# Kernel tuning notes

Hardware: AMD Instinct MI355X
Metric: run time of the kernel (lower is better)

## Reference

```python
import jax, jax.numpy as jnp
import numpy as np

N = 20000
E = 640000
IN_C, HID_C, OUT_C = 256, 256, 128
R = 8


def setup_inputs() -> dict:
    key = jax.random.key(0)
    ks = jax.random.split(key, 10)
    x = jax.random.normal(ks[0], (N, IN_C), dtype=jnp.float32)
    edge_index = jax.random.randint(ks[1], (2, E), 0, N, dtype=jnp.int64)
    edge_type = jax.random.randint(ks[2], (E,), 0, R, dtype=jnp.int64)
    s1 = 1.0 / np.sqrt(IN_C)
    s2 = 1.0 / np.sqrt(HID_C)
    W1 = jax.random.normal(ks[3], (R, IN_C, HID_C), dtype=jnp.float32) * s1
    root1 = jax.random.normal(ks[4], (IN_C, HID_C), dtype=jnp.float32) * s1
    b1 = jnp.zeros((HID_C,), dtype=jnp.float32)
    W2 = jax.random.normal(ks[5], (R, HID_C, OUT_C), dtype=jnp.float32) * s2
    root2 = jax.random.normal(ks[6], (HID_C, OUT_C), dtype=jnp.float32) * s2
    b2 = jnp.zeros((OUT_C,), dtype=jnp.float32)
    return {"x": x, "W1": W1, "root1": root1, "b1": b1,
            "W2": W2, "root2": root2, "b2": b2,
            "edge_index": edge_index, "edge_type": edge_type}


def _rgcn_conv(x, W, root, b, src, dst, etype):
    # Per-relation transform of ALL nodes: [R, N, out]
    t = jnp.einsum('ni,rio->rno', x, W)
    # Gather relation-specific messages per edge: [E, out]
    msg = t[etype, src]
    # Mean aggregation per (target node, relation), as in PyG RGCNConv (aggr='mean')
    comp = dst * R + etype  # composite segment id [E]
    cnt = jax.ops.segment_sum(jnp.ones_like(etype, dtype=x.dtype), comp,
                              num_segments=x.shape[0] * R)
    norm = 1.0 / jnp.maximum(cnt[comp], 1.0)
    agg = jax.ops.segment_sum(msg * norm[:, None], dst,
                              num_segments=x.shape[0])
    return agg + x @ root + b


def reference(x, W1, root1, b1, W2, root2, b2, edge_index, edge_type):
    src, dst = edge_index[0], edge_index[1]
    h = jax.nn.relu(_rgcn_conv(x, W1, root1, b1, src, dst, edge_type))
    return _rgcn_conv(h, W2, root2, b2, src, dst, edge_type)
```

## Files before the change

kernel.cpp:

```cpp
#include <hip/hip_runtime.h>

#define NN 20000
#define NE 640000
#define NR 8
#define NSEG (NN * NR)
#define KCAT 2304
#define KA   2048
#define CH1 256
#define CH2 128

typedef __attribute__((ext_vector_type(8))) short short8;
typedef __attribute__((ext_vector_type(4))) float f32x4;

#define AS_GLOBAL __attribute__((address_space(1)))
#define AS_LDS    __attribute__((address_space(3)))

__device__ __forceinline__ float bf2f(unsigned short u) {
    unsigned int x = ((unsigned int)u) << 16;
    return __builtin_bit_cast(float, x);
}
__device__ __forceinline__ unsigned short f2bf(float f) {
    unsigned int u = __builtin_bit_cast(unsigned int, f);
    u = (u + 0x7FFFu + ((u >> 16) & 1u)) >> 16;
    return (unsigned short)u;
}
__device__ __forceinline__ f32x4 cvt4(ushort4 v) {
    f32x4 r;
    r.x = bf2f(v.x); r.y = bf2f(v.y); r.z = bf2f(v.z); r.w = bf2f(v.w);
    return r;
}

__global__ void prologue1(const int* __restrict__ dst, const int* __restrict__ et,
                          int* __restrict__ cnt,
                          const float* __restrict__ x, unsigned short* __restrict__ xbf) {
    int gid = blockIdx.x * 256 + threadIdx.x;
    if (gid < NN * 64) {
        float4 v = reinterpret_cast<const float4*>(x)[gid];
        ushort4 o;
        o.x = f2bf(v.x); o.y = f2bf(v.y); o.z = f2bf(v.z); o.w = f2bf(v.w);
        reinterpret_cast<ushort4*>(xbf)[gid] = o;
    }
    if (gid < NE) atomicAdd(&cnt[et[gid] * NN + dst[gid]], 1);
}

__global__ void scan1(const int* __restrict__ cnt, int* __restrict__ off,
                      int* __restrict__ bsum) {
    __shared__ int s[256];
    int i = blockIdx.x * 256 + threadIdx.x;
    int v = (i < NSEG) ? cnt[i] : 0;
    s[threadIdx.x] = v;
    __syncthreads();
    for (int d = 1; d < 256; d <<= 1) {
        int t = (threadIdx.x >= d) ? s[threadIdx.x - d] : 0;
        __syncthreads();
        s[threadIdx.x] += t;
        __syncthreads();
    }
    if (i < NSEG) off[i] = s[threadIdx.x] - v;
    if (threadIdx.x == 255) bsum[blockIdx.x] = s[255];
}

__global__ __launch_bounds__(1024) void scan2(int* __restrict__ bsum, int nb) {
    __shared__ int s[1024];
    int t = threadIdx.x;
    int v = (t < nb) ? bsum[t] : 0;
    s[t] = v;
    __syncthreads();
    for (int d = 1; d < 1024; d <<= 1) {
        int tv = (t >= d) ? s[t - d] : 0;
        __syncthreads();
        s[t] += tv;
        __syncthreads();
    }
    if (t < nb) bsum[t] = s[t] - v;
}

__global__ void scan3(int* __restrict__ off, const int* __restrict__ bsum,
                      int* __restrict__ cursor) {
    int i = blockIdx.x * 256 + threadIdx.x;
    if (i < NSEG) {
        int o = off[i] + bsum[blockIdx.x];
        off[i] = o;
        cursor[i] = o;
    }
}

__global__ void bucket_kernel(const int* __restrict__ src, const int* __restrict__ dst,
                              const int* __restrict__ et, int* __restrict__ cursor,
                              int* __restrict__ ss) {
    int e = blockIdx.x * blockDim.x + threadIdx.x;
    if (e < NE) {
        int p = atomicAdd(&cursor[et[e] * NN + dst[e]], 1);
        ss[p] = src[e];
    }
}

__global__ void build_wt_all(const float* __restrict__ root1, const float* __restrict__ W1,
                             const float* __restrict__ root2, const float* __restrict__ W2,
                             unsigned short* __restrict__ W1T, unsigned short* __restrict__ W2T) {
    int i = blockIdx.x * 256 + threadIdx.x;
    if (i < CH1 * KCAT) {
        int n = i / KCAT, k = i - n * KCAT;
        float v = (k < 256) ? root1[(size_t)k * CH1 + n] : W1[(size_t)(k - 256) * CH1 + n];
        W1T[(size_t)n * KCAT + k] = f2bf(v);
    } else if (i < (CH1 + CH2) * KCAT) {
        int j = i - CH1 * KCAT;
        int n = j / KCAT, k = j - n * KCAT;
        float v = (k < 256) ? root2[(size_t)k * CH2 + n] : W2[(size_t)(k - 256) * CH2 + n];
        W2T[(size_t)n * KCAT + k] = f2bf(v);
    }
}

__global__ __launch_bounds__(256) void gather_all(const unsigned short* __restrict__ xb,
                                                  const int* __restrict__ ss,
                                                  const int* __restrict__ off,
                                                  const int* __restrict__ cnt,
                                                  unsigned short* __restrict__ A,
                                                  int n0, int rows) {
    int wid  = blockIdx.x * 4 + (threadIdx.x >> 6);
    int lane = threadIdx.x & 63;
    if (wid >= rows * NR) return;
    int n = wid >> 3;
    int r = wid & 7;
    int idx  = r * NN + (n0 + n);
    int base = off[idx];
    int c    = cnt[idx];

    f32x4 z = {0.f, 0.f, 0.f, 0.f};
    f32x4 a0 = z, a1 = z, a2 = z, a3 = z;
    int jj = 0;
    for (; jj + 4 <= c; jj += 4) {
        int s0 = ss[base + jj + 0];
        int s1 = ss[base + jj + 1];
        int s2 = ss[base + jj + 2];
        int s3 = ss[base + jj + 3];
        ushort4 v0 = reinterpret_cast<const ushort4*>(xb + (size_t)s0 * 256)[lane];
        ushort4 v1 = reinterpret_cast<const ushort4*>(xb + (size_t)s1 * 256)[lane];
        ushort4 v2 = reinterpret_cast<const ushort4*>(xb + (size_t)s2 * 256)[lane];
        ushort4 v3 = reinterpret_cast<const ushort4*>(xb + (size_t)s3 * 256)[lane];
        a0 += cvt4(v0); a1 += cvt4(v1); a2 += cvt4(v2); a3 += cvt4(v3);
    }
    int rem = c - jj;
    if (rem > 0) {
        int s0 = ss[base + jj + 0];
        int s1 = (rem > 1) ? ss[base + jj + 1] : s0;
        int s2 = (rem > 2) ? ss[base + jj + 2] : s0;
        ushort4 v0 = reinterpret_cast<const ushort4*>(xb + (size_t)s0 * 256)[lane];
        ushort4 v1 = (rem > 1) ? reinterpret_cast<const ushort4*>(xb + (size_t)s1 * 256)[lane] : make_ushort4(0,0,0,0);
        ushort4 v2 = (rem > 2) ? reinterpret_cast<const ushort4*>(xb + (size_t)s2 * 256)[lane] : make_ushort4(0,0,0,0);
        a0 += cvt4(v0);
        if (rem > 1) a1 += cvt4(v1);
        if (rem > 2) a2 += cvt4(v2);
    }
    f32x4 acc = (a0 + a1) + (a2 + a3);
    float inv = (c > 0) ? 1.f / (float)c : 0.f;
    ushort4 o;
    o.x = f2bf(acc.x * inv); o.y = f2bf(acc.y * inv);
    o.z = f2bf(acc.z * inv); o.w = f2bf(acc.w * inv);
    reinterpret_cast<ushort4*>(A + (size_t)n * KA + r * 256)[lane] = o;
}

template<int NOUT, int BN, bool RELU_BF16>
__global__ __launch_bounds__(256) void gemm_mfma(const unsigned short* __restrict__ A,
                                                 const unsigned short* __restrict__ Xsrc,
                                                 const unsigned short* __restrict__ BT,
                                                 const float* __restrict__ bias,
                                                 void* __restrict__ Cout,
                                                 int M, int mrow0) {
    constexpr int MI = 2;
    constexpr int NI = BN / 32;
    __shared__ __align__(16) unsigned short As[64 * 64];
    __shared__ __align__(16) unsigned short Bs[BN * 64];
    const int tid  = threadIdx.x;
    const int lane = tid & 63;
    const int w    = tid >> 6;
    const int wr   = w >> 1, wc = w & 1;
    const int wrow = wr * 32;
    const int wcol = wc * (NI * 16);
    const int row0 = blockIdx.x * 64;
    const int col0 = blockIdx.y * BN;

    const int srow8 = lane >> 3;
    const int skk8  = (lane & 7) * 8;
    int ra0 = row0 + w * 16 + srow8;
    int ra1 = row0 + w * 16 + 8 + srow8;
    ra0 = (ra0 < M) ? ra0 : (M - 1);
    ra1 = (ra1 < M) ? ra1 : (M - 1);
    const unsigned short* pax0 = Xsrc + (size_t)(mrow0 + ra0) * 256 + skk8;
    const unsigned short* pax1 = Xsrc + (size_t)(mrow0 + ra1) * 256 + skk8;
    const unsigned short* paa0 = A + (size_t)ra0 * KA + skk8 - 256;
    const unsigned short* paa1 = A + (size_t)ra1 * KA + skk8 - 256;
    unsigned short* lA0 = As + (w * 16) * 64;
    unsigned short* lA1 = As + (w * 16 + 8) * 64;
    constexpr int BI = BN / 32;
    const unsigned short* pb[4];
    unsigned short* lB[4];
    #pragma unroll
    for (int i = 0; i < BI; ++i) {
        int rb = (BN == 128) ? (w * 32 + i * 8) : (w * 16 + i * 8);
        pb[i] = BT + (size_t)(col0 + rb + srow8) * KCAT + skk8;
        lB[i] = Bs + (rb) * 64;
    }

    f32x4 acc[MI][NI] = {};
    const int fr = lane & 15;
    const int ka = (lane >> 4) * 8;

    for (int k0 = 0; k0 < KCAT; k0 += 64) {
        const unsigned short* p0 = (k0 < 256) ? (pax0 + k0) : (paa0 + k0);
        const unsigned short* p1 = (k0 < 256) ? (pax1 + k0) : (paa1 + k0);
        __builtin_amdgcn_global_load_lds((const AS_GLOBAL unsigned int*)p0,
                                         (AS_LDS unsigned int*)lA0, 16, 0, 0);
        __builtin_amdgcn_global_load_lds((const AS_GLOBAL unsigned int*)p1,
                                         (AS_LDS unsigned int*)lA1, 16, 0, 0);
        #pragma unroll
        for (int i = 0; i < BI; ++i)
            __builtin_amdgcn_global_load_lds((const AS_GLOBAL unsigned int*)(pb[i] + k0),
                                             (AS_LDS unsigned int*)lB[i], 16, 0, 0);
        __syncthreads();

        short8 af[MI][2], bfr[NI][2];
        #pragma unroll
        for (int i = 0; i < MI; ++i) {
            af[i][0] = *reinterpret_cast<const short8*>(&As[(wrow + i * 16 + fr) * 64 + ka]);
            af[i][1] = *reinterpret_cast<const short8*>(&As[(wrow + i * 16 + fr) * 64 + 32 + ka]);
        }
        #pragma unroll
        for (int i = 0; i < NI; ++i) {
            bfr[i][0] = *reinterpret_cast<const short8*>(&Bs[(wcol + i * 16 + fr) * 64 + ka]);
            bfr[i][1] = *reinterpret_cast<const short8*>(&Bs[(wcol + i * 16 + fr) * 64 + 32 + ka]);
        }
        #pragma unroll
        for (int s = 0; s < 2; ++s)
            #pragma unroll
            for (int mi = 0; mi < MI; ++mi)
                #pragma unroll
                for (int ni = 0; ni < NI; ++ni)
                    acc[mi][ni] = __builtin_amdgcn_mfma_f32_16x16x32_bf16(af[mi][s], bfr[ni][s], acc[mi][ni], 0, 0, 0);
        __syncthreads();
    }

    #pragma unroll
    for (int mi = 0; mi < MI; ++mi) {
        #pragma unroll
        for (int q = 0; q < 4; ++q) {
            int gm = row0 + wrow + mi * 16 + (lane >> 4) * 4 + q;
            if (gm >= M) continue;
            #pragma unroll
            for (int ni = 0; ni < NI; ++ni) {
                int gn = col0 + wcol + ni * 16 + fr;
                float v = acc[mi][ni][q] + bias[gn];
                if (RELU_BF16) {
                    v = fmaxf(v, 0.f);
                    ((unsigned short*)Cout)[(size_t)(mrow0 + gm) * NOUT + gn] = f2bf(v);
                } else {
                    ((float*)Cout)[(size_t)(mrow0 + gm) * NOUT + gn] = v;
                }
            }
        }
    }
}

extern "C" void kernel_launch(void* const* d_in, const int* in_sizes, int n_in,
                              void* d_out, int out_size, void* d_ws, size_t ws_size,
                              hipStream_t stream) {
    const float* x     = (const float*)d_in[0];
    const float* W1    = (const float*)d_in[1];
    const float* root1 = (const float*)d_in[2];
    const float* b1    = (const float*)d_in[3];
    const float* W2    = (const float*)d_in[4];
    const float* root2 = (const float*)d_in[5];
    const float* b2    = (const float*)d_in[6];
    const int*   ei    = (const int*)d_in[7];
    const int*   et    = (const int*)d_in[8];
    const int* src = ei;
    const int* dst = ei + NE;
    float* out = (float*)d_out;

    char* ws = (char*)d_ws;
    int*            cnt    = (int*)(ws + 0);
    int*            off    = (int*)(ws + 640000);
    int*            cursor = (int*)(ws + 1280000);
    int*            bsum   = (int*)(ws + 1920000);
    int*            ss     = (int*)(ws + 1923072);
    unsigned short* x_bf   = (unsigned short*)(ws + 4483072);
    unsigned short* h_bf   = (unsigned short*)(ws + 14723072);
    unsigned short* W1T    = (unsigned short*)(ws + 24963072);
    unsigned short* W2T    = (unsigned short*)(ws + 26142720);
    unsigned short* A      = (unsigned short*)(ws + 26732544);

    size_t availA = (ws_size > 26732544) ? ws_size - 26732544 : 0;
    int rowsC = (int)(availA / ((size_t)KA * 2));
    if (rowsC > NN) rowsC = NN;
    if (rowsC >= 256) rowsC &= ~127;
    if (rowsC < 1) rowsC = 1;

    const int NB = (NSEG + 255) / 256;

    hipMemsetAsync(cnt, 0, (size_t)NSEG * 4, stream);
    prologue1<<<(NN * 64 + 255) / 256, 256, 0, stream>>>(dst, et, cnt, x, x_bf);
    scan1<<<NB, 256, 0, stream>>>(cnt, off, bsum);
    scan2<<<1, 1024, 0, stream>>>(bsum, NB);
    scan3<<<NB, 256, 0, stream>>>(off, bsum, cursor);
    bucket_kernel<<<(NE + 255) / 256, 256, 0, stream>>>(src, dst, et, cursor, ss);
    build_wt_all<<<((CH1 + CH2) * KCAT + 255) / 256, 256, 0, stream>>>(root1, W1, root2, W2, W1T, W2T);

    for (int n0 = 0; n0 < NN; n0 += rowsC) {
        int rows = (NN - n0 < rowsC) ? (NN - n0) : rowsC;
        gather_all<<<(rows * NR + 3) / 4, 256, 0, stream>>>(x_bf, ss, off, cnt, A, n0, rows);
        dim3 g((rows + 63) / 64, CH1 / 128);
        gemm_mfma<CH1, 128, true><<<g, 256, 0, stream>>>(A, x_bf, W1T, b1, h_bf, rows, n0);
    }
    for (int n0 = 0; n0 < NN; n0 += rowsC) {
        int rows = (NN - n0 < rowsC) ? (NN - n0) : rowsC;
        gather_all<<<(rows * NR + 3) / 4, 256, 0, stream>>>(h_bf, ss, off, cnt, A, n0, rows);
        dim3 g((rows + 63) / 64, CH2 / 64);
        gemm_mfma<CH2, 64, false><<<g, 256, 0, stream>>>(A, h_bf, W2T, b2, out, rows, n0);
    }
}
```

Measured before the change: 419.2 us.

## Double-buffer GEMM LDS tiles and XOR-swizzle columns to avoid bank conflicts

```diff
diff --git a/kernel.cpp b/kernel.cpp
--- a/kernel.cpp
+++ b/kernel.cpp
@@ -169,8 +169,10 @@
                                                  int M, int mrow0) {
     constexpr int MI = 2;
     constexpr int NI = BN / 32;
-    __shared__ __align__(16) unsigned short As[64 * 64];
-    __shared__ __align__(16) unsigned short Bs[BN * 64];
+    constexpr int BI = BN / 32;
+    constexpr int NT = KCAT / 64;
+    __shared__ __align__(16) unsigned short As[2][64 * 64];
+    __shared__ __align__(16) unsigned short Bs[2][BN * 64];
     const int tid  = threadIdx.x;
     const int lane = tid & 63;
     const int w    = tid >> 6;
@@ -181,54 +183,69 @@
     const int col0 = blockIdx.y * BN;
 
     const int srow8 = lane >> 3;
-    const int skk8  = (lane & 7) * 8;
+    const int csw   = ((lane & 7) ^ srow8) * 8;
     int ra0 = row0 + w * 16 + srow8;
     int ra1 = row0 + w * 16 + 8 + srow8;
     ra0 = (ra0 < M) ? ra0 : (M - 1);
     ra1 = (ra1 < M) ? ra1 : (M - 1);
-    const unsigned short* pax0 = Xsrc + (size_t)(mrow0 + ra0) * 256 + skk8;
-    const unsigned short* pax1 = Xsrc + (size_t)(mrow0 + ra1) * 256 + skk8;
-    const unsigned short* paa0 = A + (size_t)ra0 * KA + skk8 - 256;
-    const unsigned short* paa1 = A + (size_t)ra1 * KA + skk8 - 256;
-    unsigned short* lA0 = As + (w * 16) * 64;
-    unsigned short* lA1 = As + (w * 16 + 8) * 64;
-    constexpr int BI = BN / 32;
+    const unsigned short* pax0 = Xsrc + (size_t)(mrow0 + ra0) * 256 + csw;
+    const unsigned short* pax1 = Xsrc + (size_t)(mrow0 + ra1) * 256 + csw;
+    const unsigned short* paa0 = A + (size_t)ra0 * KA + csw - 256;
+    const unsigned short* paa1 = A + (size_t)ra1 * KA + csw - 256;
     const unsigned short* pb[4];
-    unsigned short* lB[4];
+    int rbofs[4];
     #pragma unroll
     for (int i = 0; i < BI; ++i) {
         int rb = (BN == 128) ? (w * 32 + i * 8) : (w * 16 + i * 8);
-        pb[i] = BT + (size_t)(col0 + rb + srow8) * KCAT + skk8;
-        lB[i] = Bs + (rb) * 64;
-    }
+        rbofs[i] = rb * 64;
+        pb[i] = BT + (size_t)(col0 + rb + srow8) * KCAT + csw;
+    }
+    const int lofsA0 = (w * 16) * 64;
+    const int lofsA1 = (w * 16 + 8) * 64;
 
     f32x4 acc[MI][NI] = {};
-    const int fr = lane & 15;
-    const int ka = (lane >> 4) * 8;
-
-    for (int k0 = 0; k0 < KCAT; k0 += 64) {
+    const int fr  = lane & 15;
+    const int q   = lane >> 4;
+    const int frx = fr & 7;
+
+    auto STAGE = [&](int buf, int k0) {
         const unsigned short* p0 = (k0 < 256) ? (pax0 + k0) : (paa0 + k0);
         const unsigned short* p1 = (k0 < 256) ? (pax1 + k0) : (paa1 + k0);
         __builtin_amdgcn_global_load_lds((const AS_GLOBAL unsigned int*)p0,
-                                         (AS_LDS unsigned int*)lA0, 16, 0, 0);
+                                         (AS_LDS unsigned int*)(&As[buf][lofsA0]), 16, 0, 0);
         __builtin_amdgcn_global_load_lds((const AS_GLOBAL unsigned int*)p1,
-                                         (AS_LDS unsigned int*)lA1, 16, 0, 0);
+                                         (AS_LDS unsigned int*)(&As[buf][lofsA1]), 16, 0, 0);
         #pragma unroll
         for (int i = 0; i < BI; ++i)
             __builtin_amdgcn_global_load_lds((const AS_GLOBAL unsigned int*)(pb[i] + k0),
-                                             (AS_LDS unsigned int*)lB[i], 16, 0, 0);
-        __syncthreads();
-
+                                             (AS_LDS unsigned int*)(&Bs[buf][rbofs[i]]), 16, 0, 0);
+    };
+
+    STAGE(0, 0);
+    for (int t = 0; t < NT; ++t) {
+        if (t + 1 < NT) {
+            STAGE((t + 1) & 1, (t + 1) * 64);
+            if constexpr (BI == 4) asm volatile("s_waitcnt vmcnt(6)" ::: "memory");
+            else                   asm volatile("s_waitcnt vmcnt(4)" ::: "memory");
+        } else {
+            asm volatile("s_waitcnt vmcnt(0)" ::: "memory");
+        }
+        __builtin_amdgcn_s_barrier();
+
+        const unsigned short* Ab = &As[t & 1][0];
+        const unsigned short* Bb = &Bs[t & 1][0];
         short8 af[MI][2], bfr[NI][2];
         #pragma unroll
         for (int i = 0; i < MI; ++i) {
-            af[i][0] = *reinterpret_cast<const short8*>(&As[(wrow + i * 16 + fr) * 64 + ka]);
-            af[i][1] = *reinterpret_cast<const short8*>(&As[(wrow + i * 16 + fr) * 64 + 32 + ka]);
+            int rr = (wrow + i * 16 + fr) * 64;
+            af[i][0] = *reinterpret_cast<const short8*>(&Ab[rr + ((q ^ frx) * 8)]);
+            af[i][1] = *reinterpret_cast<const short8*>(&Ab[rr + (((4 + q) ^ frx) * 8)]);
         }
         #pragma unroll
         for (int i = 0; i < NI; ++i) {
-            bfr[i][0] = *reinterpret_cast<const short8*>(&Bs[(wcol + i * 16 + fr) * 64 + ka]);
-            bfr[i][1] = *reinterpret_cast<const short8*>(&Bs[(wcol + i * 16 + fr) * 64 + 32 + ka]);
+            int rr = (wcol + i * 16 + fr) * 64;
+            bfr[i][0] = *reinterpret_cast<const short8*>(&Bb[rr + ((q ^ frx) * 8)]);
+            bfr[i][1] = *reinterpret_cast<const short8*>(&Bb[rr + (((4 + q) ^ frx) * 8)]);
         }
         #pragma unroll
         for (int s = 0; s < 2; ++s)
@@ -237,19 +254,19 @@
                 #pragma unroll
                 for (int ni = 0; ni < NI; ++ni)
                     acc[mi][ni] = __builtin_amdgcn_mfma_f32_16x16x32_bf16(af[mi][s], bfr[ni][s], acc[mi][ni], 0, 0, 0);
-        __syncthreads();
+        __builtin_amdgcn_s_barrier();
     }
 
     #pragma unroll
     for (int mi = 0; mi < MI; ++mi) {
         #pragma unroll
-        for (int q = 0; q < 4; ++q) {
-            int gm = row0 + wrow + mi * 16 + (lane >> 4) * 4 + q;
+        for (int qq = 0; qq < 4; ++qq) {
+            int gm = row0 + wrow + mi * 16 + (lane >> 4) * 4 + qq;
             if (gm >= M) continue;
             #pragma unroll
             for (int ni = 0; ni < NI; ++ni) {
                 int gn = col0 + wcol + ni * 16 + fr;
-                float v = acc[mi][ni][q] + bias[gn];
+                float v = acc[mi][ni][qq] + bias[gn];
                 if (RELU_BF16) {
                     v = fmaxf(v, 0.f);
                     ((unsigned short*)Cout)[(size_t)(mrow0 + gm) * NOUT + gn] = f2bf(v);
```

Measured after the change: 380.6 us. 1.1x faster.
